# Kernel tuning notes

Hardware: AMD Instinct MI355X
Metric: run time of the kernel (lower is better)

Reference implementation:

```python
import jax, jax.numpy as jnp
import numpy as np

E, D_IN, D_OUT = 8, 1024, 1024
B, S = 4, 2048

def setup_inputs() -> dict:
    key = jax.random.key(0)
    k_x, k_g, k_gb, k_w = jax.random.split(key, 4)
    x = jax.random.normal(k_x, (B, S, D_IN), dtype=jnp.float32)
    gate_w = jax.random.normal(k_g, (D_IN, E), dtype=jnp.float32) * 0.02
    gate_b = jax.random.normal(k_gb, (E,), dtype=jnp.float32) * 0.02
    expert_w = jax.random.normal(k_w, (E, D_IN, D_OUT), dtype=jnp.float32) * 0.02
    return {"x": x, "gate_w": gate_w, "gate_b": gate_b, "expert_w": expert_w}

def reference(x, gate_w, gate_b, expert_w):
    # gate: softmax over experts
    gate_score = jax.nn.softmax(x @ gate_w + gate_b, axis=-1)        # [B,S,E]
    # all-expert dense GEMM: [B,S,E,out]
    expert_out = jnp.einsum('bsi,eio->bseo', x, expert_w)
    # gate-weighted combine: [B,S,out]
    out = jnp.einsum('bse,bseo->bso', gate_score, expert_out)
    return out
```

## Files before the change

### kernel.cpp

```cpp
#include <hip/hip_runtime.h>
#include <hip/hip_bf16.h>
#include <cstdint>

#define TOKENS 8192
#define DIN 1024
#define DOUT 1024
#define NE 8

typedef __bf16 bf16;
typedef __attribute__((ext_vector_type(8))) __bf16 bf16x8;
typedef __attribute__((ext_vector_type(4))) float floatx4;
typedef __attribute__((ext_vector_type(2))) float floatx2;

__device__ __forceinline__ void async16(const void* gptr, void* lptr) {
  __builtin_amdgcn_global_load_lds(
      (const __attribute__((address_space(1))) void*)gptr,
      (__attribute__((address_space(3))) void*)lptr,
      16, 0, 0);
}

__global__ __launch_bounds__(256) void prep_kernel(
    const float* __restrict__ x, const float* __restrict__ gw,
    const float* __restrict__ gb, float* __restrict__ g,
    bf16* __restrict__ xb, const float* __restrict__ w,
    bf16* __restrict__ wt) {
  __shared__ __align__(16) float smem[NE * DIN];

  if (blockIdx.x < 512) {
    const int tid = threadIdx.x;
#pragma unroll
    for (int k = 0; k < 8; ++k) {
      const int base = (k * 256 + tid) * 4;
      const floatx4 v = *(const floatx4*)(gw + base);
#pragma unroll
      for (int m = 0; m < 4; ++m) {
        const int j = base + m;
        smem[(j & 7) * DIN + (j >> 3)] = v[m];
      }
    }
    __syncthreads();

    const int lane = tid & 63;
    const int wave = tid >> 6;
#pragma unroll
    for (int tt = 0; tt < 4; ++tt) {
      const int t = blockIdx.x * 16 + wave * 4 + tt;
      const float* xr = x + (size_t)t * DIN;
      bf16* xbr = xb + (size_t)t * DIN;

      float acc[NE];
#pragma unroll
      for (int e = 0; e < NE; ++e) acc[e] = 0.f;

#pragma unroll
      for (int it = 0; it < 4; ++it) {
        const int i = it * 256 + lane * 4;
        const floatx4 xv = *(const floatx4*)(xr + i);
        union { bf16 b[4]; uint64_t u; } cv;
#pragma unroll
        for (int m = 0; m < 4; ++m) cv.b[m] = (bf16)xv[m];
        *(uint64_t*)(xbr + i) = cv.u;
#pragma unroll
        for (int e = 0; e < NE; ++e) {
          const floatx4 wv = *(const floatx4*)(smem + e * DIN + i);
          acc[e] += xv[0] * wv[0] + xv[1] * wv[1] + xv[2] * wv[2] + xv[3] * wv[3];
        }
      }
#pragma unroll
      for (int e = 0; e < NE; ++e)
#pragma unroll
        for (int off = 32; off > 0; off >>= 1)
          acc[e] += __shfl_xor(acc[e], off, 64);

      float lg[NE];
      float mx = -3.0e38f;
#pragma unroll
      for (int e = 0; e < NE; ++e) { lg[e] = acc[e] + gb[e]; mx = fmaxf(mx, lg[e]); }
      float s = 0.f;
#pragma unroll
      for (int e = 0; e < NE; ++e) { lg[e] = __expf(lg[e] - mx); s += lg[e]; }
      const float inv = 1.f / s;
      if (lane == 0) {
        floatx4 o0, o1;
#pragma unroll
        for (int e = 0; e < 4; ++e) { o0[e] = lg[e] * inv; o1[e] = lg[e + 4] * inv; }
        *(floatx4*)(g + (size_t)t * NE) = o0;
        *(floatx4*)(g + (size_t)t * NE + 4) = o1;
      }
    }
  } else {
    float (*tile)[65] = (float(*)[65])smem;
    const int b = blockIdx.x - 512;
    const int e = b >> 8;
    const int i0 = ((b >> 4) & 15) * 64;
    const int o0 = (b & 15) * 64;
    const int tid = threadIdx.x;
    const int c4 = (tid & 15) * 4;
    const int r = tid >> 4;

    const float* src = w + ((size_t)e * DIN + i0) * DOUT + o0;
#pragma unroll
    for (int rr = r; rr < 64; rr += 16) {
      const floatx4 v = *(const floatx4*)(src + (size_t)rr * DOUT + c4);
      tile[rr][c4] = v[0]; tile[rr][c4 + 1] = v[1];
      tile[rr][c4 + 2] = v[2]; tile[rr][c4 + 3] = v[3];
    }
    __syncthreads();
    bf16* dst = wt + ((size_t)e * DOUT + o0) * DIN + i0;
#pragma unroll
    for (int rr = r; rr < 64; rr += 16) {
      union { bf16 b[4]; uint64_t u; } cv;
#pragma unroll
      for (int j = 0; j < 4; ++j) cv.b[j] = (bf16)tile[c4 + j][rr];
      *(uint64_t*)(dst + (size_t)rr * DIN + c4) = cv.u;
    }
  }
}

__global__ __launch_bounds__(256, 2) void moe_gemm(
    const bf16* __restrict__ xb, const bf16* __restrict__ wt,
    const float* __restrict__ g, float* __restrict__ out) {
  __shared__ __align__(16) bf16 As[2][128 * 64];
  __shared__ __align__(16) bf16 Bs[2][128 * 64];

  const int tid = threadIdx.x;
  const int c = blockIdx.x & 7;
  const int jj = blockIdx.x >> 3;
  const int bm = (c >> 1) * 16 + (jj & 15);
  const int bn = (c & 1) * 4 + (jj >> 4);
  const int lane = tid & 63;
  const int wave = tid >> 6;
  const int wm = wave >> 1, wn = wave & 1;
  const int lr = lane & 15, lq = lane >> 4;

  const int srow = tid >> 3;
  const int scol = (((tid & 7) ^ (srow & 7)) << 3);
  const int kx = lr & 7;

  const bf16* const agp = xb + (size_t)(bm * 128 + srow) * DIN + scol;
  const bf16* const bgp = wt + (size_t)(bn * 128 + srow) * DIN + scol;

  const floatx4 fzero = {0.f, 0.f, 0.f, 0.f};
  floatx4 accF[4][4], accE[4][4];
#pragma unroll
  for (int im = 0; im < 4; ++im)
#pragma unroll
    for (int in = 0; in < 4; ++in) { accF[im][in] = fzero; accE[im][in] = fzero; }

  const int tok0 = bm * 128 + wm * 64;

  {
    bf16* const alp = &As[0][tid * 8];
    bf16* const blp = &Bs[0][tid * 8];
#pragma unroll
    for (int j = 0; j < 4; ++j)
      async16(agp + (size_t)(32 * j) * DIN, alp + j * 2048);
#pragma unroll
    for (int j = 0; j < 4; ++j)
      async16(bgp + (size_t)(32 * j) * DIN, blp + j * 2048);
  }
  __syncthreads();

  for (int t = 0; t < 128; ++t) {
    const int cur = t & 1;
    const bf16* const Ab = &As[cur][0];
    const bf16* const Bb = &Bs[cur][0];

    bf16x8 av[2][4], bv[2][4];
#pragma unroll
    for (int kk = 0; kk < 2; ++kk) {
      const int kg = ((kk * 4 + lq) ^ kx) << 3;
#pragma unroll
      for (int im = 0; im < 4; ++im)
        av[kk][im] = *(const bf16x8*)(Ab + (wm * 64 + im * 16 + lr) * 64 + kg);
#pragma unroll
      for (int in = 0; in < 4; ++in)
        bv[kk][in] = *(const bf16x8*)(Bb + (wn * 64 + in * 16 + lr) * 64 + kg);
    }

    const int t1 = t + 1;
    bf16* const alp = &As[cur ^ 1][tid * 8];
    bf16* const blp = &Bs[cur ^ 1][tid * 8];
    const size_t koff = (size_t)((t1 & 15) << 6);
    if (t1 < 128) {
#pragma unroll
      for (int j = 0; j < 4; ++j)
        async16(agp + koff + (size_t)(32 * j) * DIN, alp + j * 2048);
    }

    __builtin_amdgcn_s_setprio(1);
#pragma unroll
    for (int im = 0; im < 4; ++im)
#pragma unroll
      for (int in = 0; in < 4; ++in)
        accE[im][in] = __builtin_amdgcn_mfma_f32_16x16x32_bf16(
            av[0][im], bv[0][in], accE[im][in], 0, 0, 0);
    __builtin_amdgcn_s_setprio(0);

    if (t1 < 128) {
      const bf16* const bsrc = bgp + ((size_t)(t1 >> 4) << 20) + koff;
#pragma unroll
      for (int j = 0; j < 4; ++j)
        async16(bsrc + (size_t)(32 * j) * DIN, blp + j * 2048);
    }

    __builtin_amdgcn_s_setprio(1);
#pragma unroll
    for (int im = 0; im < 4; ++im)
#pragma unroll
      for (int in = 0; in < 4; ++in)
        accE[im][in] = __builtin_amdgcn_mfma_f32_16x16x32_bf16(
            av[1][im], bv[1][in], accE[im][in], 0, 0, 0);
    __builtin_amdgcn_s_setprio(0);

    if ((t & 15) == 15) {
      const int e = t >> 4;
#pragma unroll
      for (int im = 0; im < 4; ++im) {
        float gv[4];
#pragma unroll
        for (int r = 0; r < 4; ++r)
          gv[r] = g[(size_t)(tok0 + im * 16 + lq * 4 + r) * NE + e];
#pragma unroll
        for (int in = 0; in < 4; ++in)
#pragma unroll
          for (int r = 0; r < 4; ++r) {
            accF[im][in][r] += gv[r] * accE[im][in][r];
            accE[im][in][r] = 0.f;
          }
      }
    }

    __syncthreads();
  }

#pragma unroll
  for (int im = 0; im < 4; ++im)
#pragma unroll
    for (int in = 0; in < 4; ++in) {
      const int col = bn * 128 + wn * 64 + in * 16 + lr;
#pragma unroll
      for (int r = 0; r < 4; ++r)
        out[(size_t)(tok0 + im * 16 + lq * 4 + r) * DOUT + col] =
            accF[im][in][r];
    }
}

extern "C" void kernel_launch(void* const* d_in, const int* in_sizes, int n_in,
                              void* d_out, int out_size, void* d_ws,
                              size_t ws_size, hipStream_t stream) {
  const float* x  = (const float*)d_in[0];
  const float* gw = (const float*)d_in[1];
  const float* gb = (const float*)d_in[2];
  const float* w  = (const float*)d_in[3];
  float* out = (float*)d_out;

  char* ws = (char*)d_ws;
  float* g  = (float*)ws;
  bf16* xb  = (bf16*)(ws + 262144);
  bf16* wt  = (bf16*)(ws + 262144 + (size_t)TOKENS * DIN * 2);

  prep_kernel<<<2560, 256, 0, stream>>>(x, gw, gb, g, xb, w, wt);
  moe_gemm<<<512, 256, 0, stream>>>(xb, wt, g, out);
}
```

Measured before the change: 232.6 us.

## Load A fragments directly from global into registers and split prep kernel

The GEMM drops the LDS staging buffer for the activation tile. Each wave now loads its A fragments straight from global memory into registers, prefetching the next k-step into a second register set. The combined prep kernel is split into separate weight-transpose and gating kernels, so the transpose blocks no longer carry the gate kernel's large shared-memory allocation. Halving LDS use in the GEMM cuts barrier-guarded traffic and may allow more residency, at the cost of redundant global reads (the two wn waves load the same A rows), more registers, and one extra kernel launch.

```diff
diff --git a/kernel.cpp b/kernel.cpp
--- a/kernel.cpp
+++ b/kernel.cpp
@@ -19,108 +19,107 @@
       16, 0, 0);
 }
 
-__global__ __launch_bounds__(256) void prep_kernel(
+__global__ __launch_bounds__(256) void gate_kernel(
     const float* __restrict__ x, const float* __restrict__ gw,
     const float* __restrict__ gb, float* __restrict__ g,
-    bf16* __restrict__ xb, const float* __restrict__ w,
-    bf16* __restrict__ wt) {
+    bf16* __restrict__ xb) {
   __shared__ __align__(16) float smem[NE * DIN];
 
-  if (blockIdx.x < 512) {
-    const int tid = threadIdx.x;
-#pragma unroll
-    for (int k = 0; k < 8; ++k) {
-      const int base = (k * 256 + tid) * 4;
-      const floatx4 v = *(const floatx4*)(gw + base);
-#pragma unroll
-      for (int m = 0; m < 4; ++m) {
-        const int j = base + m;
-        smem[(j & 7) * DIN + (j >> 3)] = v[m];
+  const int tid = threadIdx.x;
+#pragma unroll
+  for (int k = 0; k < 8; ++k) {
+    const int base = (k * 256 + tid) * 4;
+    const floatx4 v = *(const floatx4*)(gw + base);
+#pragma unroll
+    for (int m = 0; m < 4; ++m) {
+      const int j = base + m;
+      smem[(j & 7) * DIN + (j >> 3)] = v[m];
+    }
+  }
+  __syncthreads();
+
+  const int lane = tid & 63;
+  const int wave = tid >> 6;
+#pragma unroll
+  for (int tt = 0; tt < 4; ++tt) {
+    const int t = blockIdx.x * 16 + wave * 4 + tt;
+    const float* xr = x + (size_t)t * DIN;
+    bf16* xbr = xb + (size_t)t * DIN;
+
+    float acc[NE];
+#pragma unroll
+    for (int e = 0; e < NE; ++e) acc[e] = 0.f;
+
+#pragma unroll
+    for (int it = 0; it < 4; ++it) {
+      const int i = it * 256 + lane * 4;
+      const floatx4 xv = *(const floatx4*)(xr + i);
+      union { bf16 b[4]; uint64_t u; } cv;
+#pragma unroll
+      for (int m = 0; m < 4; ++m) cv.b[m] = (bf16)xv[m];
+      *(uint64_t*)(xbr + i) = cv.u;
+#pragma unroll
+      for (int e = 0; e < NE; ++e) {
+        const floatx4 wv = *(const floatx4*)(smem + e * DIN + i);
+        acc[e] += xv[0] * wv[0] + xv[1] * wv[1] + xv[2] * wv[2] + xv[3] * wv[3];
       }
     }
-    __syncthreads();
-
-    const int lane = tid & 63;
-    const int wave = tid >> 6;
-#pragma unroll
-    for (int tt = 0; tt < 4; ++tt) {
-      const int t = blockIdx.x * 16 + wave * 4 + tt;
-      const float* xr = x + (size_t)t * DIN;
-      bf16* xbr = xb + (size_t)t * DIN;
-
-      float acc[NE];
-#pragma unroll
-      for (int e = 0; e < NE; ++e) acc[e] = 0.f;
-
-#pragma unroll
-      for (int it = 0; it < 4; ++it) {
-        const int i = it * 256 + lane * 4;
-        const floatx4 xv = *(const floatx4*)(xr + i);
-        union { bf16 b[4]; uint64_t u; } cv;
-#pragma unroll
-        for (int m = 0; m < 4; ++m) cv.b[m] = (bf16)xv[m];
-        *(uint64_t*)(xbr + i) = cv.u;
-#pragma unroll
-        for (int e = 0; e < NE; ++e) {
-          const floatx4 wv = *(const floatx4*)(smem + e * DIN + i);
-          acc[e] += xv[0] * wv[0] + xv[1] * wv[1] + xv[2] * wv[2] + xv[3] * wv[3];
-        }
-      }
-#pragma unroll
-      for (int e = 0; e < NE; ++e)
-#pragma unroll
-        for (int off = 32; off > 0; off >>= 1)
-          acc[e] += __shfl_xor(acc[e], off, 64);
-
-      float lg[NE];
-      float mx = -3.0e38f;
-#pragma unroll
-      for (int e = 0; e < NE; ++e) { lg[e] = acc[e] + gb[e]; mx = fmaxf(mx, lg[e]); }
-      float s = 0.f;
-#pragma unroll
-      for (int e = 0; e < NE; ++e) { lg[e] = __expf(lg[e] - mx); s += lg[e]; }
-      const float inv = 1.f / s;
-      if (lane == 0) {
-        floatx4 o0, o1;
-#pragma unroll
-        for (int e = 0; e < 4; ++e) { o0[e] = lg[e] * inv; o1[e] = lg[e + 4] * inv; }
-        *(floatx4*)(g + (size_t)t * NE) = o0;
-        *(floatx4*)(g + (size_t)t * NE + 4) = o1;
-      }
-    }
-  } else {
-    float (*tile)[65] = (float(*)[65])smem;
-    const int b = blockIdx.x - 512;
-    const int e = b >> 8;
-    const int i0 = ((b >> 4) & 15) * 64;
-    const int o0 = (b & 15) * 64;
-    const int tid = threadIdx.x;
-    const int c4 = (tid & 15) * 4;
-    const int r = tid >> 4;
-
-    const float* src = w + ((size_t)e * DIN + i0) * DOUT + o0;
-#pragma unroll
-    for (int rr = r; rr < 64; rr += 16) {
-      const floatx4 v = *(const floatx4*)(src + (size_t)rr * DOUT + c4);
-      tile[rr][c4] = v[0]; tile[rr][c4 + 1] = v[1];
-      tile[rr][c4 + 2] = v[2]; tile[rr][c4 + 3] = v[3];
-    }
-    __syncthreads();
-    bf16* dst = wt + ((size_t)e * DOUT + o0) * DIN + i0;
-#pragma unroll
-    for (int rr = r; rr < 64; rr += 16) {
-      union { bf16 b[4]; uint64_t u; } cv;
-#pragma unroll
-      for (int j = 0; j < 4; ++j) cv.b[j] = (bf16)tile[c4 + j][rr];
-      *(uint64_t*)(dst + (size_t)rr * DIN + c4) = cv.u;
-    }
+#pragma unroll
+    for (int e = 0; e < NE; ++e)
+#pragma unroll
+      for (int off = 32; off > 0; off >>= 1)
+        acc[e] += __shfl_xor(acc[e], off, 64);
+
+    float lg[NE];
+    float mx = -3.0e38f;
+#pragma unroll
+    for (int e = 0; e < NE; ++e) { lg[e] = acc[e] + gb[e]; mx = fmaxf(mx, lg[e]); }
+    float s = 0.f;
+#pragma unroll
+    for (int e = 0; e < NE; ++e) { lg[e] = __expf(lg[e] - mx); s += lg[e]; }
+    const float inv = 1.f / s;
+    if (lane == 0) {
+      floatx4 o0, o1;
+#pragma unroll
+      for (int e = 0; e < 4; ++e) { o0[e] = lg[e] * inv; o1[e] = lg[e + 4] * inv; }
+      *(floatx4*)(g + (size_t)t * NE) = o0;
+      *(floatx4*)(g + (size_t)t * NE + 4) = o1;
+    }
+  }
+}
+
+__global__ __launch_bounds__(256) void trans_kernel(
+    const float* __restrict__ w, bf16* __restrict__ wt) {
+  __shared__ __align__(16) float tile[64][65];
+  const int b = blockIdx.x;
+  const int e = b >> 8;
+  const int i0 = ((b >> 4) & 15) * 64;
+  const int o0 = (b & 15) * 64;
+  const int tid = threadIdx.x;
+  const int c4 = (tid & 15) * 4;
+  const int r = tid >> 4;
+
+  const float* src = w + ((size_t)e * DIN + i0) * DOUT + o0;
+#pragma unroll
+  for (int rr = r; rr < 64; rr += 16) {
+    const floatx4 v = *(const floatx4*)(src + (size_t)rr * DOUT + c4);
+    tile[rr][c4] = v[0]; tile[rr][c4 + 1] = v[1];
+    tile[rr][c4 + 2] = v[2]; tile[rr][c4 + 3] = v[3];
+  }
+  __syncthreads();
+  bf16* dst = wt + ((size_t)e * DOUT + o0) * DIN + i0;
+#pragma unroll
+  for (int rr = r; rr < 64; rr += 16) {
+    union { bf16 b[4]; uint64_t u; } cv;
+#pragma unroll
+    for (int j = 0; j < 4; ++j) cv.b[j] = (bf16)tile[c4 + j][rr];
+    *(uint64_t*)(dst + (size_t)rr * DIN + c4) = cv.u;
   }
 }
 
 __global__ __launch_bounds__(256, 2) void moe_gemm(
     const bf16* __restrict__ xb, const bf16* __restrict__ wt,
     const float* __restrict__ g, float* __restrict__ out) {
-  __shared__ __align__(16) bf16 As[2][128 * 64];
   __shared__ __align__(16) bf16 Bs[2][128 * 64];
 
   const int tid = threadIdx.x;
@@ -137,8 +136,8 @@
   const int scol = (((tid & 7) ^ (srow & 7)) << 3);
   const int kx = lr & 7;
 
-  const bf16* const agp = xb + (size_t)(bm * 128 + srow) * DIN + scol;
   const bf16* const bgp = wt + (size_t)(bn * 128 + srow) * DIN + scol;
+  const bf16* const abase = xb + (size_t)(bm * 128 + wm * 64 + lr) * DIN + lq * 8;
 
   const floatx4 fzero = {0.f, 0.f, 0.f, 0.f};
   floatx4 accF[4][4], accE[4][4];
@@ -150,42 +149,45 @@
   const int tok0 = bm * 128 + wm * 64;
 
   {
-    bf16* const alp = &As[0][tid * 8];
     bf16* const blp = &Bs[0][tid * 8];
-#pragma unroll
-    for (int j = 0; j < 4; ++j)
-      async16(agp + (size_t)(32 * j) * DIN, alp + j * 2048);
 #pragma unroll
     for (int j = 0; j < 4; ++j)
       async16(bgp + (size_t)(32 * j) * DIN, blp + j * 2048);
   }
+  bf16x8 avc[2][4], avn[2][4];
+#pragma unroll
+  for (int kk = 0; kk < 2; ++kk)
+#pragma unroll
+    for (int im = 0; im < 4; ++im)
+      avc[kk][im] = *(const bf16x8*)(abase + (size_t)(im * 16) * DIN + kk * 32);
   __syncthreads();
 
   for (int t = 0; t < 128; ++t) {
-    const int cur = t & 1;
-    const bf16* const Ab = &As[cur][0];
-    const bf16* const Bb = &Bs[cur][0];
-
-    bf16x8 av[2][4], bv[2][4];
+    const bf16* const Bb = &Bs[t & 1][0];
+
+    bf16x8 bv[2][4];
 #pragma unroll
     for (int kk = 0; kk < 2; ++kk) {
       const int kg = ((kk * 4 + lq) ^ kx) << 3;
 #pragma unroll
-      for (int im = 0; im < 4; ++im)
-        av[kk][im] = *(const bf16x8*)(Ab + (wm * 64 + im * 16 + lr) * 64 + kg);
-#pragma unroll
       for (int in = 0; in < 4; ++in)
         bv[kk][in] = *(const bf16x8*)(Bb + (wn * 64 + in * 16 + lr) * 64 + kg);
     }
 
     const int t1 = t + 1;
-    bf16* const alp = &As[cur ^ 1][tid * 8];
-    bf16* const blp = &Bs[cur ^ 1][tid * 8];
-    const size_t koff = (size_t)((t1 & 15) << 6);
     if (t1 < 128) {
+      const size_t koff = (size_t)((t1 & 15) << 6);
+#pragma unroll
+      for (int kk = 0; kk < 2; ++kk)
+#pragma unroll
+        for (int im = 0; im < 4; ++im)
+          avn[kk][im] = *(const bf16x8*)(abase + (size_t)(im * 16) * DIN +
+                                         koff + kk * 32);
+      const bf16* const bsrc = bgp + ((size_t)(t1 >> 4) << 20) + koff;
+      bf16* const blp = &Bs[t1 & 1][tid * 8];
 #pragma unroll
       for (int j = 0; j < 4; ++j)
-        async16(agp + koff + (size_t)(32 * j) * DIN, alp + j * 2048);
+        async16(bsrc + (size_t)(32 * j) * DIN, blp + j * 2048);
     }
 
     __builtin_amdgcn_s_setprio(1);
@@ -194,15 +196,8 @@
 #pragma unroll
       for (int in = 0; in < 4; ++in)
         accE[im][in] = __builtin_amdgcn_mfma_f32_16x16x32_bf16(
-            av[0][im], bv[0][in], accE[im][in], 0, 0, 0);
+            avc[0][im], bv[0][in], accE[im][in], 0, 0, 0);
     __builtin_amdgcn_s_setprio(0);
-
-    if (t1 < 128) {
-      const bf16* const bsrc = bgp + ((size_t)(t1 >> 4) << 20) + koff;
-#pragma unroll
-      for (int j = 0; j < 4; ++j)
-        async16(bsrc + (size_t)(32 * j) * DIN, blp + j * 2048);
-    }
 
     __builtin_amdgcn_s_setprio(1);
 #pragma unroll
@@ -210,7 +205,7 @@
 #pragma unroll
       for (int in = 0; in < 4; ++in)
         accE[im][in] = __builtin_amdgcn_mfma_f32_16x16x32_bf16(
-            av[1][im], bv[1][in], accE[im][in], 0, 0, 0);
+            avc[1][im], bv[1][in], accE[im][in], 0, 0, 0);
     __builtin_amdgcn_s_setprio(0);
 
     if ((t & 15) == 15) {
@@ -232,6 +227,12 @@
     }
 
     __syncthreads();
+
+#pragma unroll
+    for (int kk = 0; kk < 2; ++kk)
+#pragma unroll
+      for (int im = 0; im < 4; ++im)
+        avc[kk][im] = avn[kk][im];
   }
 
 #pragma unroll
@@ -260,6 +261,7 @@
   bf16* xb  = (bf16*)(ws + 262144);
   bf16* wt  = (bf16*)(ws + 262144 + (size_t)TOKENS * DIN * 2);
 
-  prep_kernel<<<2560, 256, 0, stream>>>(x, gw, gb, g, xb, w, wt);
+  trans_kernel<<<2048, 256, 0, stream>>>(w, wt);
+  gate_kernel<<<512, 256, 0, stream>>>(x, gw, gb, g, xb);
   moe_gemm<<<512, 256, 0, stream>>>(xb, wt, g, out);
 }
```

Measured after the change: 384.0 us. 1.65x slower.
